# Kernel optimization log

Measured on AMD Instinct MI355X. Metric: run time of the kernel, lower is better.

Reference implementation:

```python
import jax, jax.numpy as jnp
import numpy as np

NUM_HEADS = 16


def setup_inputs() -> dict:
    key = jax.random.key(0)
    ks = jax.random.split(key, 7)
    B, S, D, E = 4, 512, 512, 128
    H = NUM_HEADS
    return {
        "x": jax.random.normal(ks[0], (B, S, D), dtype=jnp.float32),
        "p": jax.random.normal(ks[1], (B, S, S, E), dtype=jnp.float32),
        "attention_matrix_mask": jax.random.randint(ks[2], (B, S, S), 0, 2, dtype=jnp.int32),
        "Wqkv": jax.random.normal(ks[3], (D, 3 * D), dtype=jnp.float32) * (1.0 / np.sqrt(D)),
        "bqkv": jax.random.normal(ks[4], (3 * D,), dtype=jnp.float32) * 0.02,
        "Wrqk": jax.random.normal(ks[5], (E, 2 * H), dtype=jnp.float32) * (1.0 / np.sqrt(E)),
        "brqk": jax.random.normal(ks[6], (2 * H,), dtype=jnp.float32) * 0.02,
    }


def reference(x, p, attention_matrix_mask, Wqkv, bqkv, Wrqk, brqk):
    B, S, D = x.shape
    H = NUM_HEADS
    dh = D // H
    scale = 1.0 / np.sqrt(3.0 * dh).astype(np.float32)

    # qkv projection -> [B,H,S,3*dh]
    qkv = (x @ Wqkv + bqkv).reshape(B, S, H, 3 * dh).transpose(0, 2, 1, 3)
    q, k, v = jnp.split(qkv, 3, axis=-1)  # each [B,H,S,dh]

    # edge projection -> rq, rk each [B,H,S,S]
    rqk = (p @ Wrqk + brqk).reshape(B, S, S, H, 2).transpose(0, 3, 1, 2, 4)
    rq = rqk[..., 0]
    rk = rqk[..., 1]

    # faithful to torch broadcasting: (rq * k.unsqueeze(-2)).sum(-1)
    #   = rq[b,h,i,j] * sum_d k[b,h,i,d]  (query-position-indexed k)
    ksum = k.sum(axis=-1)[..., :, None]  # [B,H,S,1]
    qsum = q.sum(axis=-1)[..., :, None]  # [B,H,S,1]
    scores = jnp.einsum("bhid,bhjd->bhij", q, k) + rq * ksum + rk * qsum

    scores = jnp.where(attention_matrix_mask[:, None, :, :] == 0, -10000.0, scores)
    probs = jax.nn.softmax(scores * scale, axis=-1)

    out = jnp.einsum("bhij,bhjd->bhid", probs, v)  # [B,H,S,dh]
    return out.transpose(0, 2, 1, 3).reshape(B, S, D)
```

## Files before the change

### kernel.cpp

```cpp
#include <hip/hip_runtime.h>
#include <hip/hip_bf16.h>
#include <hip/hip_fp16.h>

typedef __attribute__((ext_vector_type(4))) float f32x4;
typedef __attribute__((ext_vector_type(8))) __bf16 bf16x8;
typedef __attribute__((ext_vector_type(4))) __bf16 bf16x4;
typedef __attribute__((ext_vector_type(8))) _Float16 f16x8;

static __device__ __forceinline__ f32x4 mfma16(bf16x8 a, bf16x8 b, f32x4 c){
  return __builtin_amdgcn_mfma_f32_16x16x32_bf16(a, b, c, 0, 0, 0);
}

__global__ __launch_bounds__(256) void k_cvt_x(const float* __restrict__ x, __bf16* __restrict__ xbf){
  int idx = (blockIdx.x*256 + threadIdx.x)*4;
  float4 v = *reinterpret_cast<const float4*>(x + idx);
  bf16x4 o; o[0]=(__bf16)v.x; o[1]=(__bf16)v.y; o[2]=(__bf16)v.z; o[3]=(__bf16)v.w;
  *reinterpret_cast<bf16x4*>(xbf + idx) = o;
}

__global__ __launch_bounds__(256) void k_transpose_w(const float* __restrict__ W, __bf16* __restrict__ WT){
  __shared__ __align__(16) __bf16 tile[64*80];
  int bn = blockIdx.x % 24, bk = blockIdx.x / 24;
  int n0 = bn*64, k0 = bk*64;
  int t = threadIdx.x;
#pragma unroll
  for (int r=0;r<4;r++){
    int k = r*16 + (t>>4), c4 = t&15;
    float4 v = *reinterpret_cast<const float4*>(W + (size_t)(k0+k)*1536 + n0 + c4*4);
    tile[(c4*4+0)*80 + k] = (__bf16)v.x;
    tile[(c4*4+1)*80 + k] = (__bf16)v.y;
    tile[(c4*4+2)*80 + k] = (__bf16)v.z;
    tile[(c4*4+3)*80 + k] = (__bf16)v.w;
  }
  __syncthreads();
#pragma unroll
  for (int r=0;r<2;r++){
    int idx = r*256 + t;
    int n = idx>>3, kc = idx&7;
    bf16x8 v = *reinterpret_cast<bf16x8*>(&tile[n*80 + kc*8]);
    *reinterpret_cast<bf16x8*>(WT + (size_t)(n0+n)*512 + k0 + kc*8) = v;
  }
}

__global__ __launch_bounds__(256) void k_qkv(const __bf16* __restrict__ xbf, const __bf16* __restrict__ WT,
                                             const float* __restrict__ bias,
                                             __bf16* __restrict__ qbf, __bf16* __restrict__ kbf,
                                             __bf16* __restrict__ vT){
  int bid = blockIdx.x;
  int m0 = (bid/24)*64, n0 = (bid%24)*64;
  int t = threadIdx.x, w = t>>6, l = t&63;
  int wm = (w>>1)*32, wn = (w&1)*32;
  int r = l&15, q = l>>4;
  f32x4 acc00={0,0,0,0}, acc01={0,0,0,0}, acc10={0,0,0,0}, acc11={0,0,0,0};
  const __bf16* a0p = xbf + (size_t)(m0+wm+r)*512 + q*8;
  const __bf16* a1p = a0p + 16*512;
  const __bf16* b0p = WT + (size_t)(n0+wn+r)*512 + q*8;
  const __bf16* b1p = b0p + 16*512;
#pragma unroll
  for (int ks=0; ks<16; ks++){
    bf16x8 a0 = *reinterpret_cast<const bf16x8*>(a0p + ks*32);
    bf16x8 a1 = *reinterpret_cast<const bf16x8*>(a1p + ks*32);
    bf16x8 b0 = *reinterpret_cast<const bf16x8*>(b0p + ks*32);
    bf16x8 b1 = *reinterpret_cast<const bf16x8*>(b1p + ks*32);
    acc00 = mfma16(a0,b0,acc00);
    acc01 = mfma16(a0,b1,acc01);
    acc10 = mfma16(a1,b0,acc10);
    acc11 = mfma16(a1,b1,acc11);
  }
  f32x4 accs[2][2] = {{acc00,acc01},{acc10,acc11}};
#pragma unroll
  for (int mi=0;mi<2;mi++)
#pragma unroll
  for (int ni=0;ni<2;ni++){
#pragma unroll
    for (int e=0;e<4;e++){
      int row = m0 + wm + mi*16 + q*4 + e;
      int n   = n0 + wn + ni*16 + r;
      float v = accs[mi][ni][e] + bias[n];
      int bb = row>>9, s = row&511;
      int h = n/96, c = n - h*96;
      __bf16 bv = (__bf16)v;
      if (c < 32)       qbf[((size_t)(bb*16+h)*512 + s)*32 + c] = bv;
      else if (c < 64)  kbf[((size_t)(bb*16+h)*512 + s)*32 + (c-32)] = bv;
      else              vT[((size_t)(bb*16+h)*32 + (c-64))*512 + s] = bv;
    }
  }
}

__global__ __launch_bounds__(256) void k_edge(const float* __restrict__ p, const int* __restrict__ mask,
                                              const float* __restrict__ Wrqk, const float* __restrict__ brqk,
                                              const __bf16* __restrict__ qbf, const __bf16* __restrict__ kbf,
                                              _Float16* __restrict__ edge){
  __shared__ __align__(16) __bf16 WT_lds[16*128];
  __shared__ __align__(16) _Float16 sc[16*520];
  __shared__ int mask_lds[512];
  __shared__ float ksum_lds[16], qsum_lds[16], cst_lds[16];
  int bid = blockIdx.x; int b = bid>>9, i = bid&511;
  int t = threadIdx.x, w = t>>6, l = t&63;
  int r = l&15, q = l>>4;

  mask_lds[t]       = mask[(size_t)(b*512+i)*512 + t];
  mask_lds[256+t]   = mask[(size_t)(b*512+i)*512 + 256 + t];

  {
    int h = t>>4, dd = t&15;
    const __bf16* kp = kbf + ((size_t)(b*16+h)*512 + i)*32;
    const __bf16* qp = qbf + ((size_t)(b*16+h)*512 + i)*32;
    float kv = (float)kp[dd*2] + (float)kp[dd*2+1];
    float qv = (float)qp[dd*2] + (float)qp[dd*2+1];
#pragma unroll
    for (int m=1;m<16;m<<=1){ kv += __shfl_xor(kv,m); qv += __shfl_xor(qv,m); }
    if (dd==0){ ksum_lds[h]=kv; qsum_lds[h]=qv; cst_lds[h] = brqk[2*h]*kv + brqk[2*h+1]*qv; }
  }
  __syncthreads();
  {
    int idx = t*8; int h = idx>>7, e0 = idx&127;
    float ksm = ksum_lds[h], qsm = qsum_lds[h];
    bf16x8 wv;
#pragma unroll
    for (int u=0;u<8;u++)
      wv[u] = (__bf16)(Wrqk[(e0+u)*32 + 2*h]*ksm + Wrqk[(e0+u)*32 + 2*h+1]*qsm);
    int byte = (h*128 + e0)*2; byte ^= ((h&7)<<4);
    *reinterpret_cast<bf16x8*>(((char*)WT_lds) + byte) = wv;
  }
  __syncthreads();
  bf16x8 bfrag[4];
#pragma unroll
  for (int ks=0;ks<4;ks++){
    int byte = (r*128 + ks*32 + q*8)*2; byte ^= ((r&7)<<4);
    bfrag[ks] = *reinterpret_cast<bf16x8*>(((char*)WT_lds) + byte);
  }

  const float* prow = p + (size_t)(b*512+i)*65536 + (size_t)(w*16+r)*128 + q*8;
  for (int jt=0; jt<8; jt++){
    const float* pj = prow + (size_t)jt*64*128;
    f32x4 v[8];
#pragma unroll
    for (int ks=0; ks<4; ks++){
      v[2*ks]   = *reinterpret_cast<const f32x4*>(pj + ks*32);
      v[2*ks+1] = *reinterpret_cast<const f32x4*>(pj + ks*32 + 4);
    }
    f32x4 acc = {0,0,0,0};
#pragma unroll
    for (int ks=0; ks<4; ks++){
      bf16x8 a;
      a[0]=(__bf16)v[2*ks][0]; a[1]=(__bf16)v[2*ks][1];
      a[2]=(__bf16)v[2*ks][2]; a[3]=(__bf16)v[2*ks][3];
      a[4]=(__bf16)v[2*ks+1][0]; a[5]=(__bf16)v[2*ks+1][1];
      a[6]=(__bf16)v[2*ks+1][2]; a[7]=(__bf16)v[2*ks+1][3];
      acc = mfma16(a, bfrag[ks], acc);
    }
#pragma unroll
    for (int e=0;e<4;e++){
      int j = jt*64 + w*16 + q*4 + e;
      float vv = acc[e] + cst_lds[r];
      vv = mask_lds[j] ? vv : -30000.0f;
      sc[r*520 + j] = (_Float16)vv;
    }
  }
  __syncthreads();
#pragma unroll
  for (int rr=0; rr<4; rr++){
    int idx = rr*256 + t;
    int h = idx>>6, c8 = idx&63;
    uint4 vv = *reinterpret_cast<uint4*>(&sc[h*520 + c8*8]);
    *reinterpret_cast<uint4*>(edge + ((size_t)(b*16+h)*512 + i)*512 + c8*8) = vv;
  }
}

__global__ __launch_bounds__(256) void k_attn(const __bf16* __restrict__ qbf, const __bf16* __restrict__ kbf,
                                              const __bf16* __restrict__ vT, const _Float16* __restrict__ edge,
                                              float* __restrict__ out){
  __shared__ __align__(16) _Float16 sc[64*520];
  __shared__ float rowsum[64];
  int bid = blockIdx.x;
  int b = bid>>7, h = (bid>>3)&15, i0 = (bid&7)*64;
  int t = threadIdx.x, w = t>>6, l = t&63;
  int iw = w*16, r = l&15, q = l>>4;
  size_t bh = (size_t)(b*16+h);
  const __bf16* qp = qbf + bh*512*32;
  const __bf16* kp = kbf + bh*512*32;
  const __bf16* vp = vT  + bh*32*512;
  const _Float16* ep = edge + (bh*512 + i0)*512;
  const float scale = 0.1020620726159658f;

  bf16x8 qfrag = *reinterpret_cast<const bf16x8*>(qp + (size_t)(i0+iw+r)*32 + q*8);
  for (int jt=0; jt<32; jt++){
    bf16x8 kfrag = *reinterpret_cast<const bf16x8*>(kp + (size_t)(jt*16+r)*32 + q*8);
    f32x4 acc = {0,0,0,0};
    acc = mfma16(qfrag, kfrag, acc);
#pragma unroll
    for (int e=0;e<4;e++){
      int ii = iw + q*4 + e;
      int j  = jt*16 + r;
      float s = (acc[e] + (float)ep[(size_t)ii*512 + j]) * scale;
      sc[ii*520 + j] = (_Float16)s;
    }
  }
  __syncthreads();
  {
    int row = iw + r;
    float mx = -3.0e38f;
#pragma unroll
    for (int k=0;k<16;k++){
      f16x8 vv = *reinterpret_cast<f16x8*>(((char*)sc) + (size_t)row*1040 + q*256 + k*16);
#pragma unroll
      for (int u=0;u<8;u++) mx = fmaxf(mx, (float)vv[u]);
    }
    mx = fmaxf(mx, __shfl_xor(mx,16));
    mx = fmaxf(mx, __shfl_xor(mx,32));
    float sum = 0.f;
#pragma unroll
    for (int k=0;k<16;k++){
      char* addr = ((char*)sc) + (size_t)row*1040 + q*256 + k*16;
      f16x8 sv = *reinterpret_cast<f16x8*>(addr);
      bf16x8 pv;
#pragma unroll
      for (int u=0;u<8;u++){
        float ee = __expf((float)sv[u] - mx);
        sum += ee;
        pv[u] = (__bf16)ee;
      }
      *reinterpret_cast<bf16x8*>(addr) = pv;
    }
    sum += __shfl_xor(sum,16);
    sum += __shfl_xor(sum,32);
    if (q==0) rowsum[row] = sum;
  }
  __syncthreads();
  f32x4 pacc0 = {0,0,0,0}, pacc1 = {0,0,0,0};
#pragma unroll
  for (int ks=0; ks<16; ks++){
    bf16x8 pfrag = *reinterpret_cast<bf16x8*>(((char*)sc) + (size_t)(iw+r)*1040 + ks*64 + q*16);
    bf16x8 v0 = *reinterpret_cast<const bf16x8*>(vp + (size_t)(0 +r)*512 + ks*32 + q*8);
    bf16x8 v1 = *reinterpret_cast<const bf16x8*>(vp + (size_t)(16+r)*512 + ks*32 + q*8);
    pacc0 = mfma16(pfrag, v0, pacc0);
    pacc1 = mfma16(pfrag, v1, pacc1);
  }
#pragma unroll
  for (int e=0;e<4;e++){
    int ii = iw + q*4 + e;
    float inv = 1.0f / rowsum[ii];
    out[((size_t)(b*512) + i0 + ii)*512 + h*32 +      r] = pacc0[e]*inv;
    out[((size_t)(b*512) + i0 + ii)*512 + h*32 + 16 + r] = pacc1[e]*inv;
  }
}

extern "C" void kernel_launch(void* const* d_in, const int* in_sizes, int n_in,
                              void* d_out, int out_size, void* d_ws, size_t ws_size,
                              hipStream_t stream){
  const float* x    = (const float*)d_in[0];
  const float* p    = (const float*)d_in[1];
  const int*   mask = (const int*)d_in[2];
  const float* Wqkv = (const float*)d_in[3];
  const float* bqkv = (const float*)d_in[4];
  const float* Wrqk = (const float*)d_in[5];
  const float* brqk = (const float*)d_in[6];
  float* out = (float*)d_out;
  char* ws = (char*)d_ws;

  __bf16* xbf = (__bf16*)(ws + 0);
  __bf16* WT  = (__bf16*)(ws + 2097152);
  __bf16* qbf = (__bf16*)(ws + 3670016);
  __bf16* kbf = (__bf16*)(ws + 5767168);
  __bf16* vT  = (__bf16*)(ws + 7864320);
  _Float16* edge = (_Float16*)(ws + 9961472);

  k_cvt_x<<<dim3(1024), dim3(256), 0, stream>>>(x, xbf);
  k_transpose_w<<<dim3(192), dim3(256), 0, stream>>>(Wqkv, WT);
  k_qkv<<<dim3(768), dim3(256), 0, stream>>>(xbf, WT, bqkv, qbf, kbf, vT);
  k_edge<<<dim3(2048), dim3(256), 0, stream>>>(p, mask, Wrqk, brqk, qbf, kbf, edge);
  k_attn<<<dim3(512), dim3(256), 0, stream>>>(qbf, kbf, vT, edge, out);
}
```

Before: 751.8 us.

## Fuse x conversion into QKV GEMM and widen attention blocks to 512 threads

```diff
diff --git a/kernel.cpp b/kernel.cpp
--- a/kernel.cpp
+++ b/kernel.cpp
@@ -9,13 +9,6 @@
 
 static __device__ __forceinline__ f32x4 mfma16(bf16x8 a, bf16x8 b, f32x4 c){
   return __builtin_amdgcn_mfma_f32_16x16x32_bf16(a, b, c, 0, 0, 0);
-}
-
-__global__ __launch_bounds__(256) void k_cvt_x(const float* __restrict__ x, __bf16* __restrict__ xbf){
-  int idx = (blockIdx.x*256 + threadIdx.x)*4;
-  float4 v = *reinterpret_cast<const float4*>(x + idx);
-  bf16x4 o; o[0]=(__bf16)v.x; o[1]=(__bf16)v.y; o[2]=(__bf16)v.z; o[3]=(__bf16)v.w;
-  *reinterpret_cast<bf16x4*>(xbf + idx) = o;
 }
 
 __global__ __launch_bounds__(256) void k_transpose_w(const float* __restrict__ W, __bf16* __restrict__ WT){
@@ -42,7 +35,7 @@
   }
 }
 
-__global__ __launch_bounds__(256) void k_qkv(const __bf16* __restrict__ xbf, const __bf16* __restrict__ WT,
+__global__ __launch_bounds__(256) void k_qkv(const float* __restrict__ x, const __bf16* __restrict__ WT,
                                              const float* __restrict__ bias,
                                              __bf16* __restrict__ qbf, __bf16* __restrict__ kbf,
                                              __bf16* __restrict__ vT){
@@ -52,14 +45,19 @@
   int wm = (w>>1)*32, wn = (w&1)*32;
   int r = l&15, q = l>>4;
   f32x4 acc00={0,0,0,0}, acc01={0,0,0,0}, acc10={0,0,0,0}, acc11={0,0,0,0};
-  const __bf16* a0p = xbf + (size_t)(m0+wm+r)*512 + q*8;
-  const __bf16* a1p = a0p + 16*512;
+  const float* a0p = x + (size_t)(m0+wm+r)*512 + q*8;
+  const float* a1p = a0p + 16*512;
   const __bf16* b0p = WT + (size_t)(n0+wn+r)*512 + q*8;
   const __bf16* b1p = b0p + 16*512;
 #pragma unroll
   for (int ks=0; ks<16; ks++){
-    bf16x8 a0 = *reinterpret_cast<const bf16x8*>(a0p + ks*32);
-    bf16x8 a1 = *reinterpret_cast<const bf16x8*>(a1p + ks*32);
+    f32x4 u0 = *reinterpret_cast<const f32x4*>(a0p + ks*32);
+    f32x4 u1 = *reinterpret_cast<const f32x4*>(a0p + ks*32 + 4);
+    f32x4 u2 = *reinterpret_cast<const f32x4*>(a1p + ks*32);
+    f32x4 u3 = *reinterpret_cast<const f32x4*>(a1p + ks*32 + 4);
+    bf16x8 a0, a1;
+#pragma unroll
+    for (int u=0;u<4;u++){ a0[u]=(__bf16)u0[u]; a0[4+u]=(__bf16)u1[u]; a1[u]=(__bf16)u2[u]; a1[4+u]=(__bf16)u3[u]; }
     bf16x8 b0 = *reinterpret_cast<const bf16x8*>(b0p + ks*32);
     bf16x8 b1 = *reinterpret_cast<const bf16x8*>(b1p + ks*32);
     acc00 = mfma16(a0,b0,acc00);
@@ -98,6 +96,7 @@
   int bid = blockIdx.x; int b = bid>>9, i = bid&511;
   int t = threadIdx.x, w = t>>6, l = t&63;
   int r = l&15, q = l>>4;
+  const float scale = 0.1020620726159658f;
 
   mask_lds[t]       = mask[(size_t)(b*512+i)*512 + t];
   mask_lds[256+t]   = mask[(size_t)(b*512+i)*512 + 256 + t];
@@ -154,8 +153,7 @@
     for (int e=0;e<4;e++){
       int j = jt*64 + w*16 + q*4 + e;
       float vv = acc[e] + cst_lds[r];
-      vv = mask_lds[j] ? vv : -30000.0f;
-      sc[r*520 + j] = (_Float16)vv;
+      sc[r*520 + j] = (_Float16)(mask_lds[j] ? vv*scale : -3060.0f);
     }
   }
   __syncthreads();
@@ -168,7 +166,7 @@
   }
 }
 
-__global__ __launch_bounds__(256) void k_attn(const __bf16* __restrict__ qbf, const __bf16* __restrict__ kbf,
+__global__ __launch_bounds__(512) void k_attn(const __bf16* __restrict__ qbf, const __bf16* __restrict__ kbf,
                                               const __bf16* __restrict__ vT, const _Float16* __restrict__ edge,
                                               float* __restrict__ out){
   __shared__ __align__(16) _Float16 sc[64*520];
@@ -176,7 +174,8 @@
   int bid = blockIdx.x;
   int b = bid>>7, h = (bid>>3)&15, i0 = (bid&7)*64;
   int t = threadIdx.x, w = t>>6, l = t&63;
-  int iw = w*16, r = l&15, q = l>>4;
+  int r = l&15, q = l>>4;
+  int iw = (w&3)*16, half = w>>2;
   size_t bh = (size_t)(b*16+h);
   const __bf16* qp = qbf + bh*512*32;
   const __bf16* kp = kbf + bh*512*32;
@@ -185,35 +184,42 @@
   const float scale = 0.1020620726159658f;
 
   bf16x8 qfrag = *reinterpret_cast<const bf16x8*>(qp + (size_t)(i0+iw+r)*32 + q*8);
-  for (int jt=0; jt<32; jt++){
+#pragma unroll
+  for (int u=0; u<16; u++){
+    int jt = half*16 + u;
     bf16x8 kfrag = *reinterpret_cast<const bf16x8*>(kp + (size_t)(jt*16+r)*32 + q*8);
     f32x4 acc = {0,0,0,0};
     acc = mfma16(qfrag, kfrag, acc);
 #pragma unroll
-    for (int e=0;e<4;e++){
-      int ii = iw + q*4 + e;
-      int j  = jt*16 + r;
-      float s = (acc[e] + (float)ep[(size_t)ii*512 + j]) * scale;
-      sc[ii*520 + j] = (_Float16)s;
-    }
-  }
-  __syncthreads();
-  {
+    for (int e=0;e<4;e++)
+      sc[(iw + q*4 + e)*520 + jt*16 + r] = (_Float16)acc[e];
+  }
+  __syncthreads();
+
+  if (w < 4){
     int row = iw + r;
+    const _Float16* eprow = ep + (size_t)row*512 + q*128;
+    char* scrow = ((char*)sc) + (size_t)row*1040 + q*256;
     float mx = -3.0e38f;
 #pragma unroll
     for (int k=0;k<16;k++){
-      f16x8 vv = *reinterpret_cast<f16x8*>(((char*)sc) + (size_t)row*1040 + q*256 + k*16);
-#pragma unroll
-      for (int u=0;u<8;u++) mx = fmaxf(mx, (float)vv[u]);
+      f16x8 sv = *reinterpret_cast<f16x8*>(scrow + k*16);
+      f16x8 ev = *reinterpret_cast<const f16x8*>(eprow + k*8);
+      f16x8 s;
+#pragma unroll
+      for (int u=0;u<8;u++){
+        float vv = fmaf((float)sv[u], scale, (float)ev[u]);
+        mx = fmaxf(mx, vv);
+        s[u] = (_Float16)vv;
+      }
+      *reinterpret_cast<f16x8*>(scrow + k*16) = s;
     }
     mx = fmaxf(mx, __shfl_xor(mx,16));
     mx = fmaxf(mx, __shfl_xor(mx,32));
     float sum = 0.f;
 #pragma unroll
     for (int k=0;k<16;k++){
-      char* addr = ((char*)sc) + (size_t)row*1040 + q*256 + k*16;
-      f16x8 sv = *reinterpret_cast<f16x8*>(addr);
+      f16x8 sv = *reinterpret_cast<f16x8*>(scrow + k*16);
       bf16x8 pv;
 #pragma unroll
       for (int u=0;u<8;u++){
@@ -221,28 +227,27 @@
         sum += ee;
         pv[u] = (__bf16)ee;
       }
-      *reinterpret_cast<bf16x8*>(addr) = pv;
+      *reinterpret_cast<bf16x8*>(scrow + k*16) = pv;
     }
     sum += __shfl_xor(sum,16);
     sum += __shfl_xor(sum,32);
     if (q==0) rowsum[row] = sum;
   }
   __syncthreads();
-  f32x4 pacc0 = {0,0,0,0}, pacc1 = {0,0,0,0};
+
+  f32x4 pacc = {0,0,0,0};
+  const __bf16* vrow = vp + (size_t)(half*16 + r)*512;
 #pragma unroll
   for (int ks=0; ks<16; ks++){
     bf16x8 pfrag = *reinterpret_cast<bf16x8*>(((char*)sc) + (size_t)(iw+r)*1040 + ks*64 + q*16);
-    bf16x8 v0 = *reinterpret_cast<const bf16x8*>(vp + (size_t)(0 +r)*512 + ks*32 + q*8);
-    bf16x8 v1 = *reinterpret_cast<const bf16x8*>(vp + (size_t)(16+r)*512 + ks*32 + q*8);
-    pacc0 = mfma16(pfrag, v0, pacc0);
-    pacc1 = mfma16(pfrag, v1, pacc1);
+    bf16x8 v0 = *reinterpret_cast<const bf16x8*>(vrow + ks*32 + q*8);
+    pacc = mfma16(pfrag, v0, pacc);
   }
 #pragma unroll
   for (int e=0;e<4;e++){
     int ii = iw + q*4 + e;
     float inv = 1.0f / rowsum[ii];
-    out[((size_t)(b*512) + i0 + ii)*512 + h*32 +      r] = pacc0[e]*inv;
-    out[((size_t)(b*512) + i0 + ii)*512 + h*32 + 16 + r] = pacc1[e]*inv;
+    out[((size_t)(b*512) + i0 + ii)*512 + h*32 + half*16 + r] = pacc[e]*inv;
   }
 }
 
@@ -259,16 +264,14 @@
   float* out = (float*)d_out;
   char* ws = (char*)d_ws;
 
-  __bf16* xbf = (__bf16*)(ws + 0);
-  __bf16* WT  = (__bf16*)(ws + 2097152);
-  __bf16* qbf = (__bf16*)(ws + 3670016);
-  __bf16* kbf = (__bf16*)(ws + 5767168);
-  __bf16* vT  = (__bf16*)(ws + 7864320);
-  _Float16* edge = (_Float16*)(ws + 9961472);
-
-  k_cvt_x<<<dim3(1024), dim3(256), 0, stream>>>(x, xbf);
+  __bf16* WT  = (__bf16*)(ws + 0);
+  __bf16* qbf = (__bf16*)(ws + 1572864);
+  __bf16* kbf = (__bf16*)(ws + 3670016);
+  __bf16* vT  = (__bf16*)(ws + 5767168);
+  _Float16* edge = (_Float16*)(ws + 7864320);
+
   k_transpose_w<<<dim3(192), dim3(256), 0, stream>>>(Wqkv, WT);
-  k_qkv<<<dim3(768), dim3(256), 0, stream>>>(xbf, WT, bqkv, qbf, kbf, vT);
+  k_qkv<<<dim3(768), dim3(256), 0, stream>>>(x, WT, bqkv, qbf, kbf, vT);
   k_edge<<<dim3(2048), dim3(256), 0, stream>>>(p, mask, Wrqk, brqk, qbf, kbf, edge);
-  k_attn<<<dim3(512), dim3(256), 0, stream>>>(qbf, kbf, vT, edge, out);
-}
+  k_attn<<<dim3(512), dim3(512), 0, stream>>>(qbf, kbf, vT, edge, out);
+}
```

After: 763.5 us. No clear change (+1.6%).
